# Kernel optimization log

Hardware: AMD Instinct MI355X
Metric: run time of the kernel (lower is better)

## Reference

```python
import jax, jax.numpy as jnp
import numpy as np

N = 100000      # nodes
E = 1600000     # edges (avg degree 16)
F_IN = 300      # input feature dim
H = 64          # hidden channels
OUT = 20        # output classes
L = 8           # num GCN2Conv layers
ALPHA = 0.1
THETA = 0.5


def setup_inputs() -> dict:
    key = jax.random.key(0)
    ks = jax.random.split(key, 6)
    x = jax.random.normal(ks[0], (N, F_IN), jnp.float32)
    edge_index = jax.random.randint(ks[1], (2, E), 0, N, dtype=jnp.int32)
    edge_weights = jax.random.uniform(ks[2], (E,), jnp.float32)
    W_in = jax.random.normal(ks[3], (F_IN, H), jnp.float32) / np.sqrt(F_IN)
    b_in = jnp.zeros((H,), jnp.float32)
    conv_w = jax.random.normal(ks[4], (L, H, H), jnp.float32) / np.sqrt(H)
    W_out = jax.random.normal(ks[5], (H, OUT), jnp.float32) / np.sqrt(H)
    b_out = jnp.zeros((OUT,), jnp.float32)
    return dict(x=x, edge_index=edge_index, edge_weights=edge_weights,
                W_in=W_in, b_in=b_in, conv_w=conv_w, W_out=W_out, b_out=b_out)


def _gcn_norm(edge_index, edge_weights, n, dtype):
    # add self-loops with weight 1, symmetric normalization (PyG gcn_norm)
    loop = jnp.arange(n, dtype=edge_index.dtype)
    row = jnp.concatenate([edge_index[0], loop])
    col = jnp.concatenate([edge_index[1], loop])
    w = jnp.concatenate([edge_weights, jnp.ones((n,), dtype)])
    deg = jax.ops.segment_sum(w, col, num_segments=n)
    dinv = jnp.where(deg > 0, jax.lax.rsqrt(deg), 0.0).astype(dtype)
    norm = dinv[row] * w * dinv[col]
    return row, col, norm


def reference(x, edge_index, edge_weights, W_in, b_in, conv_w, W_out, b_out):
    n = x.shape[0]
    row, col, norm = _gcn_norm(edge_index, edge_weights, n, x.dtype)
    # eval mode: dropout is identity
    h = jax.nn.relu(x @ W_in + b_in)   # start_with_lin (F_IN != H)
    x0 = h
    num_layers = conv_w.shape[0]
    for l in range(num_layers):
        beta = float(np.log(THETA / (l + 1) + 1.0))
        # A_hat @ h : gather sources, weight by norm, scatter-add to targets
        agg = jax.ops.segment_sum(norm[:, None] * h[row], col, num_segments=n)
        z = (1.0 - ALPHA) * agg + ALPHA * x0  # initial-residual mixing
        h = jax.nn.relu((1.0 - beta) * z + beta * (z @ conv_w[l]))
    return h @ W_out + b_out
```

## Files before the change

kernel.cpp:

```cpp
#include <hip/hip_runtime.h>
#include <hip/hip_fp16.h>
#include <math.h>


#define HID 64
#define FIN 300
#define NOUT 20
#define ALPHA 0.1f
#define DSCALE 262144.0f
#define CNT_SHIFT 25
#define DEG_MASK 0x1FFFFFFu

typedef _Float16 f16;
typedef f16 f16x8 __attribute__((ext_vector_type(8)));
typedef float f32x4 __attribute__((ext_vector_type(4)));

__device__ __forceinline__ float wdec(unsigned v) {
    union { unsigned short u; __half h; } c;
    c.u = (unsigned short)(v >> 17);
    return __half2float(c.h);
}

__device__ __forceinline__ void unpack8(const float4& v, float* f) {
    const __half2* p = reinterpret_cast<const __half2*>(&v);
#pragma unroll
    for (int i = 0; i < 4; ++i) {
        float2 t = __half22float2(p[i]);
        f[2 * i] = t.x;
        f[2 * i + 1] = t.y;
    }
}

__global__ void zero_k(unsigned* __restrict__ p, int nwords) {
    int i = blockIdx.x * blockDim.x + threadIdx.x;
    if (i < nwords) p[i] = 0u;
}

__global__ void accum_k(const int* __restrict__ col, const float* __restrict__ w,
                        unsigned* __restrict__ packed8,
                        unsigned short* __restrict__ rank16, int e, int n) {
    int i = blockIdx.x * blockDim.x + threadIdx.x;
    if (i < e) {
        int copy = blockIdx.x & 7;
        unsigned q = (unsigned)__float2uint_rn(w[i] * DSCALE);
        unsigned old = atomicAdd(&packed8[(size_t)copy * n + col[i]],
                                 (1u << CNT_SHIFT) | q);
        rank16[i] = (unsigned short)(((old >> CNT_SHIFT) & 0xFFu) | (copy << 8));
    }
}

__global__ __launch_bounds__(1024) void unpackscan_k(const unsigned* __restrict__ packed8,
                                                     float* __restrict__ dinv,
                                                     unsigned char* __restrict__ off8,
                                                     int* __restrict__ padcnt,
                                                     int* __restrict__ bsum, int n) {
    __shared__ int s[1024];
    int t = threadIdx.x, i = blockIdx.x * 1024 + t;
    int pad = 0;
    if (i < n) {
        unsigned cnt = 0, dsum = 0;
        union { unsigned char b[8]; uint2 u2; } offs;
#pragma unroll
        for (int k = 0; k < 8; ++k) {
            unsigned v = packed8[(size_t)k * n + i];
            offs.b[k] = (unsigned char)cnt;
            cnt += (v >> CNT_SHIFT);
            dsum += (v & DEG_MASK);
        }
        float d = 1.0f + (float)dsum * (1.0f / DSCALE);
        dinv[i] = rsqrtf(d);
        reinterpret_cast<uint2*>(off8)[i] = offs.u2;
        pad = (int)((cnt + 3u) & ~3u);
        padcnt[i] = pad;
    }
    s[t] = pad;
    __syncthreads();
    for (int off = 512; off > 0; off >>= 1) {
        if (t < off) s[t] += s[t + off];
        __syncthreads();
    }
    if (t == 0) bsum[blockIdx.x] = s[0];
}

__global__ void scan2_k(int* __restrict__ bsum, int nb, int* __restrict__ rp, int n) {
    if (blockIdx.x == 0 && threadIdx.x == 0) {
        int acc = 0;
        for (int b = 0; b < nb; ++b) { int v = bsum[b]; bsum[b] = acc; acc += v; }
        rp[n] = acc;
    }
}

__global__ __launch_bounds__(1024) void scan3_k(const int* __restrict__ padcnt,
                                                const int* __restrict__ bsum,
                                                int* __restrict__ rp, int n) {
    __shared__ int s[1024];
    int t = threadIdx.x, i = blockIdx.x * 1024 + t;
    int v = (i < n) ? padcnt[i] : 0;
    s[t] = v;
    __syncthreads();
    for (int off = 1; off < 1024; off <<= 1) {
        int u = (t >= off) ? s[t - off] : 0;
        __syncthreads();
        s[t] += u;
        __syncthreads();
    }
    if (i < n) rp[i] = bsum[blockIdx.x] + s[t] - v;
}

__global__ __launch_bounds__(256) void fill_k(const int* __restrict__ row,
                                              const int* __restrict__ col,
                                              const float* __restrict__ ew,
                                              const float* __restrict__ dinv,
                                              const int* __restrict__ rp,
                                              const unsigned short* __restrict__ rank16,
                                              const unsigned char* __restrict__ off8,
                                              unsigned* __restrict__ edges,
                                              int e, int n) {
    int xcd = blockIdx.x & 7;
    int lo = (int)(((long long)n * xcd) >> 3);
    int hi = (int)(((long long)n * (xcd + 1)) >> 3);
    int nblk = gridDim.x >> 3;
    int stride = nblk * 256;
    for (int i = (blockIdx.x >> 3) * 256 + threadIdx.x; i < e; i += stride) {
        int c = col[i];
        if (c < lo || c >= hi) continue;
        int r = row[i];
        float nw = (1.0f - ALPHA) * dinv[r] * ew[i] * dinv[c];
        union { __half h; unsigned short u; } cv;
        cv.h = __float2half(nw);
        unsigned short rk = rank16[i];
        int pos = rp[c] + (int)off8[c * 8 + (rk >> 8)] + (int)(rk & 0xFFu);
        edges[pos] = ((unsigned)cv.u << 17) | (unsigned)r;
    }
}

__global__ void wt_k(const float* __restrict__ Win, f16* __restrict__ Wt) {
    int i = blockIdx.x * blockDim.x + threadIdx.x;
    if (i < 64 * 320) {
        int c = i / 320, k = i - c * 320;
        Wt[i] = (k < FIN) ? (f16)Win[k * 64 + c] : (f16)0.0f;
    }
}

__global__ __launch_bounds__(256) void gemm_in_k(const float* __restrict__ x,
                                                 const f16* __restrict__ Wt,
                                                 const float* __restrict__ bin,
                                                 __half* __restrict__ x0h, int n) {
    __shared__ f16 As[64 * 72];
    int t = threadIdx.x, lane = t & 63, wv = t >> 6;
    int node0 = blockIdx.x * 64;
    int lr = lane & 15, kg = lane >> 4;
    f32x4 acc0 = {0, 0, 0, 0}, acc1 = {0, 0, 0, 0}, acc2 = {0, 0, 0, 0}, acc3 = {0, 0, 0, 0};
    int fi = t & 15;
    for (int c = 0; c < 5; ++c) {
        __syncthreads();
#pragma unroll
        for (int it = 0; it < 4; ++it) {
            int row = (t >> 4) + it * 16;
            int rr = node0 + row;
            rr = (rr < n) ? rr : (n - 1);
            int kbase = c * 64 + fi * 4;
            float4 v = make_float4(0.f, 0.f, 0.f, 0.f);
            if (kbase < FIN)
                v = *reinterpret_cast<const float4*>(x + (size_t)rr * FIN + kbase);
            union { float2 f2; f16 h[4]; } u;
            u.h[0] = (f16)v.x; u.h[1] = (f16)v.y; u.h[2] = (f16)v.z; u.h[3] = (f16)v.w;
            *reinterpret_cast<float2*>(As + row * 72 + fi * 4) = u.f2;
        }
        __syncthreads();
#pragma unroll
        for (int ks = 0; ks < 2; ++ks) {
            f16x8 a = *(const f16x8*)(As + (wv * 16 + lr) * 72 + ks * 32 + kg * 8);
            const f16* wb = Wt + c * 64 + ks * 32 + kg * 8;
            f16x8 b0 = *(const f16x8*)(wb + (0 * 16 + lr) * 320);
            f16x8 b1 = *(const f16x8*)(wb + (1 * 16 + lr) * 320);
            f16x8 b2 = *(const f16x8*)(wb + (2 * 16 + lr) * 320);
            f16x8 b3 = *(const f16x8*)(wb + (3 * 16 + lr) * 320);
            acc0 = __builtin_amdgcn_mfma_f32_16x16x32_f16(a, b0, acc0, 0, 0, 0);
            acc1 = __builtin_amdgcn_mfma_f32_16x16x32_f16(a, b1, acc1, 0, 0, 0);
            acc2 = __builtin_amdgcn_mfma_f32_16x16x32_f16(a, b2, acc2, 0, 0, 0);
            acc3 = __builtin_amdgcn_mfma_f32_16x16x32_f16(a, b3, acc3, 0, 0, 0);
        }
    }
    float bi0 = bin[0 * 16 + lr], bi1 = bin[1 * 16 + lr];
    float bi2 = bin[2 * 16 + lr], bi3 = bin[3 * 16 + lr];
    f16 ov[4][4];
#pragma unroll
    for (int r = 0; r < 4; ++r) {
        ov[0][r] = (f16)fmaxf(acc0[r] + bi0, 0.f);
        ov[1][r] = (f16)fmaxf(acc1[r] + bi1, 0.f);
        ov[2][r] = (f16)fmaxf(acc2[r] + bi2, 0.f);
        ov[3][r] = (f16)fmaxf(acc3[r] + bi3, 0.f);
    }
    __syncthreads();
#pragma unroll
    for (int cg = 0; cg < 4; ++cg)
#pragma unroll
        for (int r = 0; r < 4; ++r)
            As[(wv * 16 + kg * 4 + r) * 72 + cg * 16 + lr] = ov[cg][r];
    __syncthreads();
#pragma unroll
    for (int it = 0; it < 2; ++it) {
        int idx = t + it * 256;
        int row = idx >> 3, ch = idx & 7;
        int node = node0 + row;
        if (node < n)
            ((float4*)(x0h + (size_t)node * 64))[ch] =
                *reinterpret_cast<const float4*>(As + row * 72 + ch * 8);
    }
}

__global__ __launch_bounds__(256) void layer_k(const int* __restrict__ rp,
                                               const unsigned* __restrict__ edges,
                                               const float* __restrict__ dinv,
                                               const __half* __restrict__ x0h,
                                               const __half* __restrict__ hin,
                                               __half* __restrict__ hout,
                                               const float* __restrict__ Wl,
                                               float beta, int n) {
    __shared__ f16 As[64 * 72];
    __shared__ f16 Bs[64 * 72];
    int t = threadIdx.x, lane = t & 63, wv = t >> 6;
    int node0 = blockIdx.x * 64;
    for (int i = t; i < 4096; i += 256) {
        int k = i >> 6, c = i & 63;
        Bs[c * 72 + k] = (f16)Wl[i];
    }
    int g = lane >> 3, c8 = lane & 7;
#pragma unroll
    for (int pass = 0; pass < 2; ++pass) {
        int row = pass * 32 + wv * 8 + g;
        int node = node0 + row;
        int nd = (node < n) ? node : (n - 1);
        int j = rp[nd], end = (node < n) ? rp[nd + 1] : j;
        float a0[8], a1[8], a2[8], a3[8];
#pragma unroll
        for (int i = 0; i < 8; ++i) { a0[i] = 0.f; a1[i] = 0.f; a2[i] = 0.f; a3[i] = 0.f; }
        while (__any(j < end)) {
            bool v = j < end;
            uint4 e4 = *reinterpret_cast<const uint4*>(edges + (v ? j : 0));
            float w0 = v ? wdec(e4.x) : 0.f;
            float w1 = v ? wdec(e4.y) : 0.f;
            float w2 = v ? wdec(e4.z) : 0.f;
            float w3 = v ? wdec(e4.w) : 0.f;
            float4 r0 = ((const float4*)(hin + (size_t)(e4.x & 0x1FFFF) * 64))[c8];
            float4 r1 = ((const float4*)(hin + (size_t)(e4.y & 0x1FFFF) * 64))[c8];
            float4 r2 = ((const float4*)(hin + (size_t)(e4.z & 0x1FFFF) * 64))[c8];
            float4 r3 = ((const float4*)(hin + (size_t)(e4.w & 0x1FFFF) * 64))[c8];
            float f0[8], f1[8], f2[8], f3[8];
            unpack8(r0, f0);
            unpack8(r1, f1);
            unpack8(r2, f2);
            unpack8(r3, f3);
#pragma unroll
            for (int i = 0; i < 8; ++i) {
                a0[i] = fmaf(w0, f0[i], a0[i]);
                a1[i] = fmaf(w1, f1[i], a1[i]);
                a2[i] = fmaf(w2, f2[i], a2[i]);
                a3[i] = fmaf(w3, f3[i], a3[i]);
            }
            j += 4;
        }
        float di = dinv[nd];
        float c1 = (1.0f - ALPHA) * di * di;
        float4 hs4 = ((const float4*)(hin + (size_t)nd * 64))[c8];
        float4 xs4 = ((const float4*)(x0h + (size_t)nd * 64))[c8];
        float hf[8], xf[8];
        unpack8(hs4, hf);
        unpack8(xs4, xf);
        f16x8 zv8;
#pragma unroll
        for (int i = 0; i < 8; ++i)
            zv8[i] = (f16)fmaf(ALPHA, xf[i],
                               fmaf(c1, hf[i], (a0[i] + a1[i]) + (a2[i] + a3[i])));
        *(f16x8*)(As + row * 72 + c8 * 8) = zv8;
    }
    __syncthreads();
    int lr = lane & 15, kg = lane >> 4;
    f32x4 acc0 = {0, 0, 0, 0}, acc1 = {0, 0, 0, 0}, acc2 = {0, 0, 0, 0}, acc3 = {0, 0, 0, 0};
    f16x8 af0 = *(const f16x8*)(As + (wv * 16 + lr) * 72 + kg * 8);
    f16x8 af1 = *(const f16x8*)(As + (wv * 16 + lr) * 72 + 32 + kg * 8);
    {
        f16x8 b0 = *(const f16x8*)(Bs + (0 * 16 + lr) * 72 + kg * 8);
        f16x8 b1 = *(const f16x8*)(Bs + (0 * 16 + lr) * 72 + 32 + kg * 8);
        acc0 = __builtin_amdgcn_mfma_f32_16x16x32_f16(af0, b0, acc0, 0, 0, 0);
        acc0 = __builtin_amdgcn_mfma_f32_16x16x32_f16(af1, b1, acc0, 0, 0, 0);
    }
    {
        f16x8 b0 = *(const f16x8*)(Bs + (1 * 16 + lr) * 72 + kg * 8);
        f16x8 b1 = *(const f16x8*)(Bs + (1 * 16 + lr) * 72 + 32 + kg * 8);
        acc1 = __builtin_amdgcn_mfma_f32_16x16x32_f16(af0, b0, acc1, 0, 0, 0);
        acc1 = __builtin_amdgcn_mfma_f32_16x16x32_f16(af1, b1, acc1, 0, 0, 0);
    }
    {
        f16x8 b0 = *(const f16x8*)(Bs + (2 * 16 + lr) * 72 + kg * 8);
        f16x8 b1 = *(const f16x8*)(Bs + (2 * 16 + lr) * 72 + 32 + kg * 8);
        acc2 = __builtin_amdgcn_mfma_f32_16x16x32_f16(af0, b0, acc2, 0, 0, 0);
        acc2 = __builtin_amdgcn_mfma_f32_16x16x32_f16(af1, b1, acc2, 0, 0, 0);
    }
    {
        f16x8 b0 = *(const f16x8*)(Bs + (3 * 16 + lr) * 72 + kg * 8);
        f16x8 b1 = *(const f16x8*)(Bs + (3 * 16 + lr) * 72 + 32 + kg * 8);
        acc3 = __builtin_amdgcn_mfma_f32_16x16x32_f16(af0, b0, acc3, 0, 0, 0);
        acc3 = __builtin_amdgcn_mfma_f32_16x16x32_f16(af1, b1, acc3, 0, 0, 0);
    }
    float omb = 1.0f - beta;
    f16 ov[4][4];
#pragma unroll
    for (int cg = 0; cg < 4; ++cg) {
        f32x4 acc = (cg == 0) ? acc0 : (cg == 1) ? acc1 : (cg == 2) ? acc2 : acc3;
        int col = cg * 16 + lr;
#pragma unroll
        for (int r = 0; r < 4; ++r) {
            float zv = (float)As[(wv * 16 + kg * 4 + r) * 72 + col];
            ov[cg][r] = (f16)fmaxf(fmaf(beta, acc[r], omb * zv), 0.f);
        }
    }
    __syncthreads();
#pragma unroll
    for (int cg = 0; cg < 4; ++cg)
#pragma unroll
        for (int r = 0; r < 4; ++r)
            As[(wv * 16 + kg * 4 + r) * 72 + cg * 16 + lr] = ov[cg][r];
    __syncthreads();
#pragma unroll
    for (int it = 0; it < 2; ++it) {
        int idx = t + it * 256;
        int row = idx >> 3, ch = idx & 7;
        int node = node0 + row;
        if (node < n)
            ((float4*)(hout + (size_t)node * 64))[ch] =
                *reinterpret_cast<const float4*>(As + row * 72 + ch * 8);
    }
}

__global__ __launch_bounds__(256) void gemm_out_k(const __half* __restrict__ h,
                                                  const float* __restrict__ Wout,
                                                  const float* __restrict__ bout,
                                                  float* __restrict__ out, int n) {
    __shared__ float hs[64][65];
    __shared__ float Ws[64 * NOUT];
    __shared__ float bs[NOUT];
    int t = threadIdx.x;
    for (int i = t; i < 64 * NOUT; i += 256) Ws[i] = Wout[i];
    if (t < NOUT) bs[t] = bout[t];
    int base = blockIdx.x * 64;
    int lim = min(64, n - base);
    for (int i = t; i < 64 * 32; i += 256) {
        int r = i >> 5, c2 = (i & 31) * 2;
        float2 v = make_float2(0.f, 0.f);
        if (r < lim) {
            __half2 hv = reinterpret_cast<const __half2*>(
                h + (size_t)(base + r) * 64)[i & 31];
            v = __half22float2(hv);
        }
        hs[r][c2] = v.x;
        hs[r][c2 + 1] = v.y;
    }
    __syncthreads();
#pragma unroll
    for (int q = 0; q < 5; ++q) {
        int of = t + 256 * q;
        int nd = of / NOUT, o = of - nd * NOUT;
        float acc = bs[o];
#pragma unroll
        for (int k = 0; k < 64; ++k) acc = fmaf(hs[nd][k], Ws[k * NOUT + o], acc);
        if (nd < lim) out[(size_t)(base + nd) * NOUT + o] = acc;
    }
}

extern "C" void kernel_launch(void* const* d_in, const int* in_sizes, int n_in,
                              void* d_out, int out_size, void* d_ws, size_t ws_size,
                              hipStream_t stream) {
    const float* x    = (const float*)d_in[0];
    const int*   ei   = (const int*)d_in[1];
    const float* ew   = (const float*)d_in[2];
    const float* Win  = (const float*)d_in[3];
    const float* bin  = (const float*)d_in[4];
    const float* cw   = (const float*)d_in[5];
    const float* Wout = (const float*)d_in[6];
    const float* bout = (const float*)d_in[7];

    const int n = in_sizes[0] / FIN;
    const int e = in_sizes[2];
    const int L = in_sizes[5] / (HID * HID);
    const int* row = ei;
    const int* col = ei + e;
    const int epadmax = e + 3 * n + 64;

    size_t off = 0;
    auto alloc = [&](size_t bytes) -> char* {
        char* q = (char*)d_ws + off;
        off = (off + bytes + 255) & ~(size_t)255;
        return q;
    };
    __half* x0h  = (__half*)alloc((size_t)n * HID * 2);
    __half* hA   = (__half*)alloc((size_t)n * HID * 2);
    __half* hB   = (__half*)alloc((size_t)n * HID * 2);
    unsigned* edges = (unsigned*)alloc((size_t)epadmax * 4);
    unsigned short* rank16 = (unsigned short*)alloc((size_t)e * 2);
    unsigned* packed8 = (unsigned*)alloc((size_t)8 * n * 4);
    unsigned char* off8 = (unsigned char*)alloc((size_t)n * 8);
    float* dinv  = (float*)alloc((size_t)n * 4);
    int*   padcnt= (int*)alloc((size_t)n * 4);
    int*   rp    = (int*)alloc((size_t)(n + 1) * 4);
    int*   bsum  = (int*)alloc(1024 * 4);
    f16*   Wt    = (f16*)alloc((size_t)64 * 320 * 2);

    const int nb = (n + 1023) / 1024;
    const int ntile = (n + 63) / 64;

    zero_k<<<(8 * n + 255) / 256, 256, 0, stream>>>(packed8, 8 * n);
    zero_k<<<(epadmax + 255) / 256, 256, 0, stream>>>(edges, epadmax);
    accum_k<<<(e + 255) / 256, 256, 0, stream>>>(col, ew, packed8, rank16, e, n);
    unpackscan_k<<<nb, 1024, 0, stream>>>(packed8, dinv, off8, padcnt, bsum, n);
    scan2_k<<<1, 1, 0, stream>>>(bsum, nb, rp, n);
    scan3_k<<<nb, 1024, 0, stream>>>(padcnt, bsum, rp, n);
    fill_k<<<1024, 256, 0, stream>>>(row, col, ew, dinv, rp, rank16, off8, edges, e, n);

    wt_k<<<(64 * 320 + 255) / 256, 256, 0, stream>>>(Win, Wt);
    gemm_in_k<<<ntile, 256, 0, stream>>>(x, Wt, bin, x0h, n);

    const __half* hin = x0h;
    __half* hout = hA;
    for (int l = 0; l < L; ++l) {
        float beta = (float)log(0.5 / (double)(l + 1) + 1.0);
        layer_k<<<ntile, 256, 0, stream>>>(rp, edges, dinv, x0h, hin, hout,
                                           cw + (size_t)l * HID * HID, beta, n);
        hin = hout;
        hout = (hout == hA) ? hB : hA;
    }
    gemm_out_k<<<(n + 63) / 64, 256, 0, stream>>>(hin, Wout, bout, (float*)d_out, n);
}
```

Before: 523.5 us.

## Pack edge records, parallelize block scan, prefetch GEMM input, fuse output projection

accum_k now writes a packed 8-byte record per edge (col, copy, rank, row, fp16 weight), so fill_k makes one coalesced read instead of reading row, col, ew and rank16 separately. scan2_k becomes a single-wavefront shuffle scan instead of one serial thread. gemm_in_k loads the next x chunk into registers before running the MFMA on the current chunk, and the aggregation loop skips inactive lanes with a branch instead of clamped loads. The last layer computes the output projection in-kernel with MFMA, which removes the gemm_out launch and one write and reread of h. The trade-offs are a larger edge staging buffer and the edge weight rounded to fp16 before normalization.

```diff
diff --git a/kernel.cpp b/kernel.cpp
--- a/kernel.cpp
+++ b/kernel.cpp
@@ -36,16 +36,22 @@
     if (i < nwords) p[i] = 0u;
 }
 
-__global__ void accum_k(const int* __restrict__ col, const float* __restrict__ w,
+__global__ void accum_k(const int* __restrict__ row, const int* __restrict__ col,
+                        const float* __restrict__ w,
                         unsigned* __restrict__ packed8,
-                        unsigned short* __restrict__ rank16, int e, int n) {
+                        uint2* __restrict__ rec, int e, int n) {
     int i = blockIdx.x * blockDim.x + threadIdx.x;
     if (i < e) {
         int copy = blockIdx.x & 7;
-        unsigned q = (unsigned)__float2uint_rn(w[i] * DSCALE);
-        unsigned old = atomicAdd(&packed8[(size_t)copy * n + col[i]],
-                                 (1u << CNT_SHIFT) | q);
-        rank16[i] = (unsigned short)(((old >> CNT_SHIFT) & 0xFFu) | (copy << 8));
+        int c = col[i], r = row[i];
+        float wv = w[i];
+        unsigned q = (unsigned)__float2uint_rn(wv * DSCALE);
+        unsigned old = atomicAdd(&packed8[(size_t)copy * n + c], (1u << CNT_SHIFT) | q);
+        unsigned rank = (old >> CNT_SHIFT) & 0xFFu;
+        union { __half h; unsigned short u; } cv;
+        cv.h = __float2half(wv);
+        rec[i] = make_uint2((unsigned)c | ((unsigned)copy << 17) | (rank << 20),
+                            (unsigned)r | ((unsigned)cv.u << 17));
     }
 }
 
@@ -83,11 +89,21 @@
 }
 
 __global__ void scan2_k(int* __restrict__ bsum, int nb, int* __restrict__ rp, int n) {
-    if (blockIdx.x == 0 && threadIdx.x == 0) {
-        int acc = 0;
-        for (int b = 0; b < nb; ++b) { int v = bsum[b]; bsum[b] = acc; acc += v; }
-        rp[n] = acc;
-    }
+    int lane = threadIdx.x;
+    int acc = 0;
+    for (int base = 0; base < nb; base += 64) {
+        int idx = base + lane;
+        int orig = (idx < nb) ? bsum[idx] : 0;
+        int v = orig;
+#pragma unroll
+        for (int d = 1; d < 64; d <<= 1) {
+            int u = __shfl_up(v, d);
+            if (lane >= d) v += u;
+        }
+        if (idx < nb) bsum[idx] = acc + v - orig;
+        acc += __shfl(v, 63);
+    }
+    if (lane == 0) rp[n] = acc;
 }
 
 __global__ __launch_bounds__(1024) void scan3_k(const int* __restrict__ padcnt,
@@ -107,12 +123,9 @@
     if (i < n) rp[i] = bsum[blockIdx.x] + s[t] - v;
 }
 
-__global__ __launch_bounds__(256) void fill_k(const int* __restrict__ row,
-                                              const int* __restrict__ col,
-                                              const float* __restrict__ ew,
+__global__ __launch_bounds__(256) void fill_k(const uint2* __restrict__ rec,
                                               const float* __restrict__ dinv,
                                               const int* __restrict__ rp,
-                                              const unsigned short* __restrict__ rank16,
                                               const unsigned char* __restrict__ off8,
                                               unsigned* __restrict__ edges,
                                               int e, int n) {
@@ -122,14 +135,18 @@
     int nblk = gridDim.x >> 3;
     int stride = nblk * 256;
     for (int i = (blockIdx.x >> 3) * 256 + threadIdx.x; i < e; i += stride) {
-        int c = col[i];
+        uint2 rc = rec[i];
+        int c = (int)(rc.x & 0x1FFFFu);
         if (c < lo || c >= hi) continue;
-        int r = row[i];
-        float nw = (1.0f - ALPHA) * dinv[r] * ew[i] * dinv[c];
+        int r = (int)(rc.y & 0x1FFFFu);
+        union { unsigned short u; __half h; } ev;
+        ev.u = (unsigned short)(rc.y >> 17);
+        float nw = (1.0f - ALPHA) * dinv[r] * __half2float(ev.h) * dinv[c];
         union { __half h; unsigned short u; } cv;
         cv.h = __float2half(nw);
-        unsigned short rk = rank16[i];
-        int pos = rp[c] + (int)off8[c * 8 + (rk >> 8)] + (int)(rk & 0xFFu);
+        int copy = (int)((rc.x >> 17) & 7u);
+        int rank = (int)((rc.x >> 20) & 0xFFu);
+        int pos = rp[c] + (int)off8[c * 8 + copy] + rank;
         edges[pos] = ((unsigned)cv.u << 17) | (unsigned)r;
     }
 }
@@ -150,24 +167,36 @@
     int t = threadIdx.x, lane = t & 63, wv = t >> 6;
     int node0 = blockIdx.x * 64;
     int lr = lane & 15, kg = lane >> 4;
+    int fi = t & 15, rowbase = t >> 4;
     f32x4 acc0 = {0, 0, 0, 0}, acc1 = {0, 0, 0, 0}, acc2 = {0, 0, 0, 0}, acc3 = {0, 0, 0, 0};
-    int fi = t & 15;
-    for (int c = 0; c < 5; ++c) {
-        __syncthreads();
+    float4 xr[4];
+
+    auto loadchunk = [&](int c) {
 #pragma unroll
         for (int it = 0; it < 4; ++it) {
-            int row = (t >> 4) + it * 16;
+            int row = rowbase + it * 16;
             int rr = node0 + row;
             rr = (rr < n) ? rr : (n - 1);
             int kbase = c * 64 + fi * 4;
-            float4 v = make_float4(0.f, 0.f, 0.f, 0.f);
+            xr[it] = make_float4(0.f, 0.f, 0.f, 0.f);
             if (kbase < FIN)
-                v = *reinterpret_cast<const float4*>(x + (size_t)rr * FIN + kbase);
+                xr[it] = *reinterpret_cast<const float4*>(x + (size_t)rr * FIN + kbase);
+        }
+    };
+    loadchunk(0);
+
+    for (int c = 0; c < 5; ++c) {
+        __syncthreads();
+#pragma unroll
+        for (int it = 0; it < 4; ++it) {
+            int row = rowbase + it * 16;
             union { float2 f2; f16 h[4]; } u;
-            u.h[0] = (f16)v.x; u.h[1] = (f16)v.y; u.h[2] = (f16)v.z; u.h[3] = (f16)v.w;
+            u.h[0] = (f16)xr[it].x; u.h[1] = (f16)xr[it].y;
+            u.h[2] = (f16)xr[it].z; u.h[3] = (f16)xr[it].w;
             *reinterpret_cast<float2*>(As + row * 72 + fi * 4) = u.f2;
         }
         __syncthreads();
+        if (c < 4) loadchunk(c + 1);
 #pragma unroll
         for (int ks = 0; ks < 2; ++ks) {
             f16x8 a = *(const f16x8*)(As + (wv * 16 + lr) * 72 + ks * 32 + kg * 8);
@@ -217,7 +246,10 @@
                                                const __half* __restrict__ hin,
                                                __half* __restrict__ hout,
                                                const float* __restrict__ Wl,
-                                               float beta, int n) {
+                                               float beta, int n,
+                                               const float* __restrict__ Wout,
+                                               const float* __restrict__ bout,
+                                               float* __restrict__ out) {
     __shared__ f16 As[64 * 72];
     __shared__ f16 Bs[64 * 72];
     int t = threadIdx.x, lane = t & 63, wv = t >> 6;
@@ -237,27 +269,25 @@
 #pragma unroll
         for (int i = 0; i < 8; ++i) { a0[i] = 0.f; a1[i] = 0.f; a2[i] = 0.f; a3[i] = 0.f; }
         while (__any(j < end)) {
-            bool v = j < end;
-            uint4 e4 = *reinterpret_cast<const uint4*>(edges + (v ? j : 0));
-            float w0 = v ? wdec(e4.x) : 0.f;
-            float w1 = v ? wdec(e4.y) : 0.f;
-            float w2 = v ? wdec(e4.z) : 0.f;
-            float w3 = v ? wdec(e4.w) : 0.f;
-            float4 r0 = ((const float4*)(hin + (size_t)(e4.x & 0x1FFFF) * 64))[c8];
-            float4 r1 = ((const float4*)(hin + (size_t)(e4.y & 0x1FFFF) * 64))[c8];
-            float4 r2 = ((const float4*)(hin + (size_t)(e4.z & 0x1FFFF) * 64))[c8];
-            float4 r3 = ((const float4*)(hin + (size_t)(e4.w & 0x1FFFF) * 64))[c8];
-            float f0[8], f1[8], f2[8], f3[8];
-            unpack8(r0, f0);
-            unpack8(r1, f1);
-            unpack8(r2, f2);
-            unpack8(r3, f3);
-#pragma unroll
-            for (int i = 0; i < 8; ++i) {
-                a0[i] = fmaf(w0, f0[i], a0[i]);
-                a1[i] = fmaf(w1, f1[i], a1[i]);
-                a2[i] = fmaf(w2, f2[i], a2[i]);
-                a3[i] = fmaf(w3, f3[i], a3[i]);
+            if (j < end) {
+                uint4 e4 = *reinterpret_cast<const uint4*>(edges + j);
+                float w0 = wdec(e4.x), w1 = wdec(e4.y), w2 = wdec(e4.z), w3 = wdec(e4.w);
+                float4 r0 = ((const float4*)(hin + (size_t)(e4.x & 0x1FFFF) * 64))[c8];
+                float4 r1 = ((const float4*)(hin + (size_t)(e4.y & 0x1FFFF) * 64))[c8];
+                float4 r2 = ((const float4*)(hin + (size_t)(e4.z & 0x1FFFF) * 64))[c8];
+                float4 r3 = ((const float4*)(hin + (size_t)(e4.w & 0x1FFFF) * 64))[c8];
+                float f0[8], f1[8], f2[8], f3[8];
+                unpack8(r0, f0);
+                unpack8(r1, f1);
+                unpack8(r2, f2);
+                unpack8(r3, f3);
+#pragma unroll
+                for (int i = 0; i < 8; ++i) {
+                    a0[i] = fmaf(w0, f0[i], a0[i]);
+                    a1[i] = fmaf(w1, f1[i], a1[i]);
+                    a2[i] = fmaf(w2, f2[i], a2[i]);
+                    a3[i] = fmaf(w3, f3[i], a3[i]);
+                }
             }
             j += 4;
         }
@@ -323,49 +353,42 @@
         for (int r = 0; r < 4; ++r)
             As[(wv * 16 + kg * 4 + r) * 72 + cg * 16 + lr] = ov[cg][r];
     __syncthreads();
-#pragma unroll
-    for (int it = 0; it < 2; ++it) {
-        int idx = t + it * 256;
-        int row = idx >> 3, ch = idx & 7;
-        int node = node0 + row;
-        if (node < n)
-            ((float4*)(hout + (size_t)node * 64))[ch] =
-                *reinterpret_cast<const float4*>(As + row * 72 + ch * 8);
-    }
-}
-
-__global__ __launch_bounds__(256) void gemm_out_k(const __half* __restrict__ h,
-                                                  const float* __restrict__ Wout,
-                                                  const float* __restrict__ bout,
-                                                  float* __restrict__ out, int n) {
-    __shared__ float hs[64][65];
-    __shared__ float Ws[64 * NOUT];
-    __shared__ float bs[NOUT];
-    int t = threadIdx.x;
-    for (int i = t; i < 64 * NOUT; i += 256) Ws[i] = Wout[i];
-    if (t < NOUT) bs[t] = bout[t];
-    int base = blockIdx.x * 64;
-    int lim = min(64, n - base);
-    for (int i = t; i < 64 * 32; i += 256) {
-        int r = i >> 5, c2 = (i & 31) * 2;
-        float2 v = make_float2(0.f, 0.f);
-        if (r < lim) {
-            __half2 hv = reinterpret_cast<const __half2*>(
-                h + (size_t)(base + r) * 64)[i & 31];
-            v = __half22float2(hv);
-        }
-        hs[r][c2] = v.x;
-        hs[r][c2 + 1] = v.y;
-    }
-    __syncthreads();
-#pragma unroll
-    for (int q = 0; q < 5; ++q) {
-        int of = t + 256 * q;
-        int nd = of / NOUT, o = of - nd * NOUT;
-        float acc = bs[o];
-#pragma unroll
-        for (int k = 0; k < 64; ++k) acc = fmaf(hs[nd][k], Ws[k * NOUT + o], acc);
-        if (nd < lim) out[(size_t)(base + nd) * NOUT + o] = acc;
+
+    if (!Wout) {
+#pragma unroll
+        for (int it = 0; it < 2; ++it) {
+            int idx = t + it * 256;
+            int row = idx >> 3, ch = idx & 7;
+            int node = node0 + row;
+            if (node < n)
+                ((float4*)(hout + (size_t)node * 64))[ch] =
+                    *reinterpret_cast<const float4*>(As + row * 72 + ch * 8);
+        }
+    } else {
+        for (int i = t; i < 32 * 64; i += 256) {
+            int c = i >> 6, k = i & 63;
+            Bs[c * 72 + k] = (c < NOUT) ? (f16)Wout[k * NOUT + c] : (f16)0.0f;
+        }
+        __syncthreads();
+        f16x8 ha0 = *(const f16x8*)(As + (wv * 16 + lr) * 72 + kg * 8);
+        f16x8 ha1 = *(const f16x8*)(As + (wv * 16 + lr) * 72 + 32 + kg * 8);
+#pragma unroll
+        for (int ct = 0; ct < 2; ++ct) {
+            f32x4 oacc = {0, 0, 0, 0};
+            f16x8 b0 = *(const f16x8*)(Bs + (ct * 16 + lr) * 72 + kg * 8);
+            f16x8 b1 = *(const f16x8*)(Bs + (ct * 16 + lr) * 72 + 32 + kg * 8);
+            oacc = __builtin_amdgcn_mfma_f32_16x16x32_f16(ha0, b0, oacc, 0, 0, 0);
+            oacc = __builtin_amdgcn_mfma_f32_16x16x32_f16(ha1, b1, oacc, 0, 0, 0);
+            int col = ct * 16 + lr;
+            if (col < NOUT) {
+                float bo = bout[col];
+#pragma unroll
+                for (int r = 0; r < 4; ++r) {
+                    int node = node0 + wv * 16 + kg * 4 + r;
+                    if (node < n) out[(size_t)node * NOUT + col] = oacc[r] + bo;
+                }
+            }
+        }
     }
 }
 
@@ -398,7 +421,7 @@
     __half* hA   = (__half*)alloc((size_t)n * HID * 2);
     __half* hB   = (__half*)alloc((size_t)n * HID * 2);
     unsigned* edges = (unsigned*)alloc((size_t)epadmax * 4);
-    unsigned short* rank16 = (unsigned short*)alloc((size_t)e * 2);
+    uint2* rec   = (uint2*)alloc((size_t)e * 8);
     unsigned* packed8 = (unsigned*)alloc((size_t)8 * n * 4);
     unsigned char* off8 = (unsigned char*)alloc((size_t)n * 8);
     float* dinv  = (float*)alloc((size_t)n * 4);
@@ -412,11 +435,11 @@
 
     zero_k<<<(8 * n + 255) / 256, 256, 0, stream>>>(packed8, 8 * n);
     zero_k<<<(epadmax + 255) / 256, 256, 0, stream>>>(edges, epadmax);
-    accum_k<<<(e + 255) / 256, 256, 0, stream>>>(col, ew, packed8, rank16, e, n);
+    accum_k<<<(e + 255) / 256, 256, 0, stream>>>(row, col, ew, packed8, rec, e, n);
     unpackscan_k<<<nb, 1024, 0, stream>>>(packed8, dinv, off8, padcnt, bsum, n);
-    scan2_k<<<1, 1, 0, stream>>>(bsum, nb, rp, n);
+    scan2_k<<<1, 64, 0, stream>>>(bsum, nb, rp, n);
     scan3_k<<<nb, 1024, 0, stream>>>(padcnt, bsum, rp, n);
-    fill_k<<<1024, 256, 0, stream>>>(row, col, ew, dinv, rp, rank16, off8, edges, e, n);
+    fill_k<<<1024, 256, 0, stream>>>(rec, dinv, rp, off8, edges, e, n);
 
     wt_k<<<(64 * 320 + 255) / 256, 256, 0, stream>>>(Win, Wt);
     gemm_in_k<<<ntile, 256, 0, stream>>>(x, Wt, bin, x0h, n);
@@ -425,10 +448,13 @@
     __half* hout = hA;
     for (int l = 0; l < L; ++l) {
         float beta = (float)log(0.5 / (double)(l + 1) + 1.0);
+        bool last = (l == L - 1);
         layer_k<<<ntile, 256, 0, stream>>>(rp, edges, dinv, x0h, hin, hout,
-                                           cw + (size_t)l * HID * HID, beta, n);
+                                           cw + (size_t)l * HID * HID, beta, n,
+                                           last ? Wout : nullptr,
+                                           last ? bout : nullptr,
+                                           last ? (float*)d_out : nullptr);
         hin = hout;
         hout = (hout == hA) ? hB : hA;
     }
-    gemm_out_k<<<(n + 63) / 64, 256, 0, stream>>>(hin, Wout, bout, (float*)d_out, n);
-}
+}
```

Result: faster. 492.0 us (-6.0%).
